# Optimization experiments

Hardware: AMD Instinct MI355X
Metric: run time of the kernel (lower is better)

Reference implementation:

```python
import jax, jax.numpy as jnp
import numpy as np

N = 100000  # nodes
E = 1600000  # edges

def gcn_layer(x, W, b, src, tgt, ew):
    # support = x @ W + b ; messages gathered at src, weighted scatter-sum into tgt
    h = x @ W + b                      # [N, F_out]
    msg = h[src] * ew[:, None]         # [E, F_out]
    return jax.ops.segment_sum(msg, tgt, num_segments=N)  # [N, F_out]

def setup_inputs() -> dict:
    key = jax.random.key(0)
    ks = jax.random.split(key, 12)
    nfeat, nhid, nclass = 256, 128, 40
    x = jax.random.normal(ks[0], (N, nfeat), dtype=jnp.float32)
    src = jax.random.randint(ks[1], (E,), 0, N)
    tgt = jax.random.randint(ks[2], (E,), 0, N)
    edge_weight = jax.random.uniform(ks[3], (E,), dtype=jnp.float32)
    def w(k, fi, fo):
        return jax.random.normal(k, (fi, fo), dtype=jnp.float32) / np.sqrt(fi)
    return {
        "x": x, "src": src, "tgt": tgt, "edge_weight": edge_weight,
        "W0": w(ks[4], nfeat, nhid), "b0": jnp.zeros((nhid,), jnp.float32),
        "W1": w(ks[5], nhid, nhid),  "b1": jnp.zeros((nhid,), jnp.float32),
        "W2": w(ks[6], nhid, nhid),  "b2": jnp.zeros((nhid,), jnp.float32),
        "W3": w(ks[7], nhid, nclass),"b3": jnp.zeros((nclass,), jnp.float32),
    }

def reference(x, src, tgt, edge_weight, W0, b0, W1, b1, W2, b2, W3, b3):
    # RESK2 with nlayers=4, eval mode (dropout = identity).
    # x0 = relu(gc0); r = x0; x1 = relu(gc1); x2 = relu(gc2) + r; out = log_softmax(gc3)
    x0 = jax.nn.relu(gcn_layer(x, W0, b0, src, tgt, edge_weight))
    r = x0
    x1 = jax.nn.relu(gcn_layer(x0, W1, b1, src, tgt, edge_weight))
    x2 = jax.nn.relu(gcn_layer(x1, W2, b2, src, tgt, edge_weight)) + r
    logits = gcn_layer(x2, W3, b3, src, tgt, edge_weight)
    return jax.nn.log_softmax(logits, axis=1)
```

## Files before the change

kernel.cpp:

```cpp
#include <hip/hip_runtime.h>
#include <hip/hip_bf16.h>


typedef __attribute__((ext_vector_type(8))) short short8;
typedef __attribute__((ext_vector_type(4))) float float4v;

#define SC_SHIFT 8
#define SC_NODES 256
#define FILL_CAP 12288
#define SRC_MASK 0x1FFFF

static __device__ __forceinline__ float bf2f_lo(unsigned int v) {
    return __uint_as_float(v << 16);
}
static __device__ __forceinline__ float bf2f_hi(unsigned int v) {
    return __uint_as_float(v & 0xffff0000u);
}
static __device__ __forceinline__ unsigned short f2bf(float f) {
    unsigned int u = __float_as_uint(f);
    u = (u + 0x7fffu + ((u >> 16) & 1u)) >> 16;
    return (unsigned short)u;
}
static __device__ __forceinline__ unsigned int packbf(float a, float b) {
    return (unsigned int)f2bf(a) | ((unsigned int)f2bf(b) << 16);
}
static __device__ __forceinline__ float pw_w(unsigned int pe) {
    return __uint_as_float((pe >> 17) << 16);
}

static __device__ __forceinline__ void acc8(float* acc, uint4 v, float wt) {
    acc[0] = fmaf(bf2f_lo(v.x), wt, acc[0]);
    acc[1] = fmaf(bf2f_hi(v.x), wt, acc[1]);
    acc[2] = fmaf(bf2f_lo(v.y), wt, acc[2]);
    acc[3] = fmaf(bf2f_hi(v.y), wt, acc[3]);
    acc[4] = fmaf(bf2f_lo(v.z), wt, acc[4]);
    acc[5] = fmaf(bf2f_hi(v.z), wt, acc[5]);
    acc[6] = fmaf(bf2f_lo(v.w), wt, acc[6]);
    acc[7] = fmaf(bf2f_hi(v.w), wt, acc[7]);
}
static __device__ __forceinline__ void acc4(float* acc, uint2 v, float wt) {
    acc[0] = fmaf(bf2f_lo(v.x), wt, acc[0]);
    acc[1] = fmaf(bf2f_hi(v.x), wt, acc[1]);
    acc[2] = fmaf(bf2f_lo(v.y), wt, acc[2]);
    acc[3] = fmaf(bf2f_hi(v.y), wt, acc[3]);
}

__global__ __launch_bounds__(256) void k_count(const int* __restrict__ tgt,
                                               int* __restrict__ chunkTot,
                                               int E, int NSC) {
    __shared__ int hist[512];
    const int tid = threadIdx.x;
    hist[tid] = 0;
    hist[tid + 256] = 0;
    __syncthreads();
#pragma unroll
    for (int r = 0; r < 4; r++) {
        int e = blockIdx.x * 4096 + r * 1024 + tid * 4;
        if (e + 3 < E) {
            int4 tv = *(const int4*)&tgt[e];
            atomicAdd(&hist[tv.x >> SC_SHIFT], 1);
            atomicAdd(&hist[tv.y >> SC_SHIFT], 1);
            atomicAdd(&hist[tv.z >> SC_SHIFT], 1);
            atomicAdd(&hist[tv.w >> SC_SHIFT], 1);
        } else {
            for (int j = 0; j < 4; j++)
                if (e + j < E) atomicAdd(&hist[tgt[e + j] >> SC_SHIFT], 1);
        }
    }
    __syncthreads();
    for (int i = tid; i < NSC; i += 256) {
        int c = hist[i];
        if (c) atomicAdd(&chunkTot[i], c);
    }
}

__global__ __launch_bounds__(512) void k_scanB(const int* __restrict__ chunkTot,
                                               int* __restrict__ chunkStart,
                                               int* __restrict__ chunkCur,
                                               int E, int NSC) {
    __shared__ int sm[512];
    const int tid = threadIdx.x;
    int v = (tid < NSC) ? chunkTot[tid] : 0;
    sm[tid] = v;
    __syncthreads();
    for (int off = 1; off < 512; off <<= 1) {
        int t = (tid >= off) ? sm[tid - off] : 0;
        __syncthreads();
        sm[tid] += t;
        __syncthreads();
    }
    int excl = sm[tid] - v;
    if (tid < NSC) {
        chunkStart[tid] = excl;
        chunkCur[tid * 32] = excl;
    }
    if (tid == 0) chunkStart[NSC] = E;
}

__global__ __launch_bounds__(512) void k_bucket(const int* __restrict__ src,
                                                const int* __restrict__ tgt,
                                                const float* __restrict__ ew,
                                                int* __restrict__ chunkCur,
                                                unsigned int* __restrict__ st_pw,
                                                unsigned char* __restrict__ st_t8,
                                                int E) {
    __shared__ int cnt[512];
    __shared__ int rk[512];
    __shared__ int bbase[512];
    const int tid = threadIdx.x;
    cnt[tid] = 0;
    rk[tid] = 0;
    __syncthreads();

    int t16[16];
    unsigned int p16[16];
#pragma unroll
    for (int r = 0; r < 4; r++) {
        int e = blockIdx.x * 8192 + r * 2048 + tid * 4;
        if (e + 3 < E) {
            int4 tv = *(const int4*)&tgt[e];
            int4 sv = *(const int4*)&src[e];
            float4 wv = *(const float4*)&ew[e];
            t16[r * 4 + 0] = tv.x; t16[r * 4 + 1] = tv.y;
            t16[r * 4 + 2] = tv.z; t16[r * 4 + 3] = tv.w;
            p16[r * 4 + 0] = ((unsigned int)f2bf(wv.x) << 17) | (unsigned int)sv.x;
            p16[r * 4 + 1] = ((unsigned int)f2bf(wv.y) << 17) | (unsigned int)sv.y;
            p16[r * 4 + 2] = ((unsigned int)f2bf(wv.z) << 17) | (unsigned int)sv.z;
            p16[r * 4 + 3] = ((unsigned int)f2bf(wv.w) << 17) | (unsigned int)sv.w;
        } else {
            for (int j = 0; j < 4; j++) {
                int ee = e + j;
                t16[r * 4 + j] = (ee < E) ? tgt[ee] : -1;
                p16[r * 4 + j] = (ee < E)
                    ? (((unsigned int)f2bf(ew[ee]) << 17) | (unsigned int)src[ee])
                    : 0u;
            }
        }
    }
#pragma unroll
    for (int j = 0; j < 16; j++)
        if (t16[j] >= 0) atomicAdd(&cnt[t16[j] >> SC_SHIFT], 1);
    __syncthreads();
    {
        int c = cnt[tid];
        bbase[tid] = c ? atomicAdd(&chunkCur[tid * 32], c) : 0;
    }
    __syncthreads();
#pragma unroll
    for (int j = 0; j < 16; j++) {
        if (t16[j] >= 0) {
            int c = t16[j] >> SC_SHIFT;
            int pos = bbase[c] + atomicAdd(&rk[c], 1);
            st_pw[pos] = p16[j];
            st_t8[pos] = (unsigned char)(t16[j] & (SC_NODES - 1));
        }
    }
}

__global__ __launch_bounds__(256) void k_fill2(const unsigned int* __restrict__ st_pw,
                                               const unsigned char* __restrict__ st_t8,
                                               const int* __restrict__ chunkStart,
                                               int* __restrict__ rowptr,
                                               unsigned int* __restrict__ perm,
                                               int N, int E, int NSC) {
    __shared__ int lhist[SC_NODES];
    __shared__ int lcur[SC_NODES];
    __shared__ unsigned int ledge[FILL_CAP];
    const int tid = threadIdx.x;
    const int b = blockIdx.x;
    const int n0 = b << SC_SHIFT;
    const int nlocal = min(SC_NODES, N - n0);
    const int sstart = chunkStart[b];
    const int send = chunkStart[b + 1];
    const int cnt = send - sstart;

    lhist[tid] = 0;
    __syncthreads();
    for (int e = sstart + tid; e < send; e += 256)
        atomicAdd(&lhist[st_t8[e]], 1);
    __syncthreads();
    int v = lhist[tid];
    __syncthreads();
    lhist[tid] = v;
    __syncthreads();
    for (int off = 1; off < 256; off <<= 1) {
        int t = (tid >= off) ? lhist[tid - off] : 0;
        __syncthreads();
        lhist[tid] += t;
        __syncthreads();
    }
    int excl = lhist[tid] - v;
    if (tid < nlocal) rowptr[n0 + tid] = sstart + excl;
    if (b == NSC - 1 && tid == 0) rowptr[N] = E;
    lcur[tid] = excl;
    __syncthreads();

    if (cnt <= FILL_CAP) {
        for (int e = sstart + tid; e < send; e += 256) {
            int lt = st_t8[e];
            int pos = atomicAdd(&lcur[lt], 1);
            ledge[pos] = st_pw[e];
        }
        __syncthreads();
        for (int i = tid; i < cnt; i += 256) perm[sstart + i] = ledge[i];
    } else {
        for (int e = sstart + tid; e < send; e += 256) {
            int lt = st_t8[e];
            int pos = atomicAdd(&lcur[lt], 1);
            perm[sstart + pos] = st_pw[e];
        }
    }
}

__global__ __launch_bounds__(256) void k_wtrans_all(
    const float* __restrict__ W0, const float* __restrict__ W1,
    const float* __restrict__ W2, const float* __restrict__ W3,
    unsigned short* __restrict__ Wt0, unsigned short* __restrict__ Wt1,
    unsigned short* __restrict__ Wt2, unsigned short* __restrict__ Wt3,
    int* __restrict__ chunkTot) {
    int idx = blockIdx.x * 256 + threadIdx.x;
    if (idx < 512) chunkTot[idx] = 0;
    if (idx < 32768) {
        int c = idx >> 8, k = idx & 255;
        Wt0[idx] = f2bf(W0[k * 128 + c]);
    } else if (idx < 49152) {
        int i = idx - 32768;
        int c = i >> 7, k = i & 127;
        Wt1[i] = f2bf(W1[k * 128 + c]);
    } else if (idx < 65536) {
        int i = idx - 49152;
        int c = i >> 7, k = i & 127;
        Wt2[i] = f2bf(W2[k * 128 + c]);
    } else if (idx < 71680) {
        int i = idx - 65536;
        int c = i >> 7, k = i & 127;
        Wt3[i] = (c < 40) ? f2bf(W3[k * 40 + c]) : 0;
    }
}

template <int K, int AF32>
__global__ __launch_bounds__(256) void k_gemm_mfma(const void* __restrict__ Av,
                                                   const unsigned short* __restrict__ Wt,
                                                   const float* __restrict__ bias,
                                                   unsigned short* __restrict__ C, int N) {
    __shared__ unsigned short As[128 * 40];
    __shared__ unsigned short Bs[128 * 40];
    __shared__ float bsh[128];
    const unsigned short* A16 = (const unsigned short*)Av;
    const float* A32 = (const float*)Av;
    const int tid = threadIdx.x;
    const int wave = tid >> 6, lane = tid & 63;
    const int quad = lane >> 4, l15 = lane & 15;
    const int rowBase = blockIdx.x * 128;

    if (tid < 128) bsh[tid] = bias[tid];

    const int r0 = tid >> 2, kc0 = tid & 3;
    const int r1 = (256 + tid) >> 2, kc1 = kc0;
    int rg0 = rowBase + r0; rg0 = rg0 < N ? rg0 : N - 1;
    int rg1 = rowBase + r1; rg1 = rg1 < N ? rg1 : N - 1;

    uint4 pa[2], pb[2];
    auto load_step = [&](int k0) {
        if (AF32) {
            float4 f0 = *(const float4*)&A32[(size_t)rg0 * K + k0 + kc0 * 8];
            float4 f1 = *(const float4*)&A32[(size_t)rg0 * K + k0 + kc0 * 8 + 4];
            pa[0].x = packbf(f0.x, f0.y); pa[0].y = packbf(f0.z, f0.w);
            pa[0].z = packbf(f1.x, f1.y); pa[0].w = packbf(f1.z, f1.w);
            float4 g0 = *(const float4*)&A32[(size_t)rg1 * K + k0 + kc1 * 8];
            float4 g1 = *(const float4*)&A32[(size_t)rg1 * K + k0 + kc1 * 8 + 4];
            pa[1].x = packbf(g0.x, g0.y); pa[1].y = packbf(g0.z, g0.w);
            pa[1].z = packbf(g1.x, g1.y); pa[1].w = packbf(g1.z, g1.w);
        } else {
            pa[0] = *(const uint4*)&A16[(size_t)rg0 * K + k0 + kc0 * 8];
            pa[1] = *(const uint4*)&A16[(size_t)rg1 * K + k0 + kc1 * 8];
        }
        pb[0] = *(const uint4*)&Wt[(size_t)r0 * K + k0 + kc0 * 8];
        pb[1] = *(const uint4*)&Wt[(size_t)r1 * K + k0 + kc1 * 8];
    };

    const float4v z = {0.f, 0.f, 0.f, 0.f};
    float4v acc[2][8];
#pragma unroll
    for (int i = 0; i < 2; i++)
#pragma unroll
        for (int j = 0; j < 8; j++) acc[i][j] = z;

    load_step(0);
    for (int k0 = 0; k0 < K; k0 += 32) {
        *(uint4*)&As[r0 * 40 + kc0 * 8] = pa[0];
        *(uint4*)&As[r1 * 40 + kc1 * 8] = pa[1];
        *(uint4*)&Bs[r0 * 40 + kc0 * 8] = pb[0];
        *(uint4*)&Bs[r1 * 40 + kc1 * 8] = pb[1];
        __syncthreads();
        if (k0 + 32 < K) load_step(k0 + 32);

        short8 a0 = *(const short8*)&As[(wave * 32 + l15) * 40 + quad * 8];
        short8 a1 = *(const short8*)&As[(wave * 32 + 16 + l15) * 40 + quad * 8];
#pragma unroll
        for (int c = 0; c < 8; c++) {
            short8 b = *(const short8*)&Bs[(c * 16 + l15) * 40 + quad * 8];
            acc[0][c] = __builtin_amdgcn_mfma_f32_16x16x32_bf16(b, a0, acc[0][c], 0, 0, 0);
            acc[1][c] = __builtin_amdgcn_mfma_f32_16x16x32_bf16(b, a1, acc[1][c], 0, 0, 0);
        }
        __syncthreads();
    }

#pragma unroll
    for (int rt = 0; rt < 2; rt++) {
        int row = rowBase + wave * 32 + rt * 16 + l15;
        if (row < N) {
#pragma unroll
            for (int c = 0; c < 8; c++) {
                int colBase = c * 16 + quad * 4;
                float4 bv = *(const float4*)&bsh[colBase];
                uint2 o;
                o.x = packbf(acc[rt][c][0] + bv.x, acc[rt][c][1] + bv.y);
                o.y = packbf(acc[rt][c][2] + bv.z, acc[rt][c][3] + bv.w);
                *(uint2*)&C[(size_t)row * 128 + colBase] = o;
            }
        }
    }
}

__global__ __launch_bounds__(256) void k_gemm40_mfma(const unsigned short* __restrict__ A,
                                                     const unsigned short* __restrict__ Wt3,
                                                     const float* __restrict__ bias,
                                                     unsigned short* __restrict__ C, int N) {
    __shared__ unsigned short As[128 * 40];
    __shared__ unsigned short Bs[48 * 136];
    __shared__ float bsh[48];
    const int tid = threadIdx.x;
    const int wave = tid >> 6, lane = tid & 63;
    const int quad = lane >> 4, l15 = lane & 15;
    const int rowBase = blockIdx.x * 128;

    if (tid < 48) bsh[tid] = (tid < 40) ? bias[tid] : 0.f;
    for (int t = tid; t < 48 * 16; t += 256) {
        int r = t >> 4, kc = t & 15;
        uint4 v = *(const uint4*)&Wt3[r * 128 + kc * 8];
        *(uint4*)&Bs[r * 136 + kc * 8] = v;
    }

    const int r0 = tid >> 2, kc0 = tid & 3;
    const int r1 = r0 + 64;
    int rg0 = rowBase + r0; rg0 = rg0 < N ? rg0 : N - 1;
    int rg1 = rowBase + r1; rg1 = rg1 < N ? rg1 : N - 1;

    uint4 pa[2];
    auto load_step = [&](int k0) {
        pa[0] = *(const uint4*)&A[(size_t)rg0 * 128 + k0 + kc0 * 8];
        pa[1] = *(const uint4*)&A[(size_t)rg1 * 128 + k0 + kc0 * 8];
    };

    const float4v z = {0.f, 0.f, 0.f, 0.f};
    float4v acc[2][3];
#pragma unroll
    for (int i = 0; i < 2; i++)
#pragma unroll
        for (int j = 0; j < 3; j++) acc[i][j] = z;

    load_step(0);
    for (int k0 = 0; k0 < 128; k0 += 32) {
        *(uint4*)&As[r0 * 40 + kc0 * 8] = pa[0];
        *(uint4*)&As[r1 * 40 + kc0 * 8] = pa[1];
        __syncthreads();
        if (k0 + 32 < 128) load_step(k0 + 32);

        short8 a0 = *(const short8*)&As[(wave * 32 + l15) * 40 + quad * 8];
        short8 a1 = *(const short8*)&As[(wave * 32 + 16 + l15) * 40 + quad * 8];
#pragma unroll
        for (int c = 0; c < 3; c++) {
            short8 b = *(const short8*)&Bs[(c * 16 + l15) * 136 + k0 + quad * 8];
            acc[0][c] = __builtin_amdgcn_mfma_f32_16x16x32_bf16(b, a0, acc[0][c], 0, 0, 0);
            acc[1][c] = __builtin_amdgcn_mfma_f32_16x16x32_bf16(b, a1, acc[1][c], 0, 0, 0);
        }
        __syncthreads();
    }

#pragma unroll
    for (int rt = 0; rt < 2; rt++) {
        int row = rowBase + wave * 32 + rt * 16 + l15;
        if (row < N) {
#pragma unroll
            for (int c = 0; c < 3; c++) {
                int colBase = c * 16 + quad * 4;
                float4 bv = *(const float4*)&bsh[colBase];
                uint2 o;
                o.x = packbf(acc[rt][c][0] + bv.x, acc[rt][c][1] + bv.y);
                o.y = packbf(acc[rt][c][2] + bv.z, acc[rt][c][3] + bv.w);
                *(uint2*)&C[(size_t)row * 64 + colBase] = o;
            }
        }
    }
}

__global__ __launch_bounds__(256) void k_agg128(const unsigned short* __restrict__ h,
                                                const int* __restrict__ rowptr,
                                                const unsigned int* __restrict__ perm,
                                                const unsigned short* __restrict__ resid,
                                                unsigned short* __restrict__ out, int N) {
    int node = (blockIdx.x * 256 + threadIdx.x) >> 6;
    if (node >= N) return;
    const int lane = threadIdx.x & 63;
    const int g = lane >> 4, l = lane & 15;
    const int beg = rowptr[node], end = rowptr[node + 1];
    const int last = end - 1;

    float acc[8] = {};
    for (int base = beg; base < end; base += 16) {
        int e0 = base + g, e1 = base + 4 + g, e2 = base + 8 + g, e3 = base + 12 + g;
        unsigned int p0 = perm[e0 <= last ? e0 : last];
        unsigned int p1 = perm[e1 <= last ? e1 : last];
        unsigned int p2 = perm[e2 <= last ? e2 : last];
        unsigned int p3 = perm[e3 <= last ? e3 : last];
        uint4 a0 = *(const uint4*)&h[(size_t)(p0 & SRC_MASK) * 128 + l * 8];
        uint4 a1 = *(const uint4*)&h[(size_t)(p1 & SRC_MASK) * 128 + l * 8];
        uint4 a2 = *(const uint4*)&h[(size_t)(p2 & SRC_MASK) * 128 + l * 8];
        uint4 a3 = *(const uint4*)&h[(size_t)(p3 & SRC_MASK) * 128 + l * 8];
        float w0 = e0 <= last ? pw_w(p0) : 0.f;
        float w1 = e1 <= last ? pw_w(p1) : 0.f;
        float w2 = e2 <= last ? pw_w(p2) : 0.f;
        float w3 = e3 <= last ? pw_w(p3) : 0.f;
        acc8(acc, a0, w0);
        acc8(acc, a1, w1);
        acc8(acc, a2, w2);
        acc8(acc, a3, w3);
    }

#pragma unroll
    for (int i = 0; i < 8; i++) {
        acc[i] += __shfl_xor(acc[i], 16);
        acc[i] += __shfl_xor(acc[i], 32);
    }

    if (g == 0) {
#pragma unroll
        for (int i = 0; i < 8; i++) acc[i] = fmaxf(acc[i], 0.f);
        if (resid) {
            uint4 rv = *(const uint4*)&resid[(size_t)node * 128 + l * 8];
            acc[0] += bf2f_lo(rv.x); acc[1] += bf2f_hi(rv.x);
            acc[2] += bf2f_lo(rv.y); acc[3] += bf2f_hi(rv.y);
            acc[4] += bf2f_lo(rv.z); acc[5] += bf2f_hi(rv.z);
            acc[6] += bf2f_lo(rv.w); acc[7] += bf2f_hi(rv.w);
        }
        uint4 o;
        o.x = packbf(acc[0], acc[1]);
        o.y = packbf(acc[2], acc[3]);
        o.z = packbf(acc[4], acc[5]);
        o.w = packbf(acc[6], acc[7]);
        *(uint4*)&out[(size_t)node * 128 + l * 8] = o;
    }
}

__global__ __launch_bounds__(256) void k_agg40_lsm(const unsigned short* __restrict__ h,
                                                   const int* __restrict__ rowptr,
                                                   const unsigned int* __restrict__ perm,
                                                   float* __restrict__ out, int N) {
    int node = (blockIdx.x * 256 + threadIdx.x) >> 6;
    if (node >= N) return;
    const int lane = threadIdx.x & 63;
    const int g = lane >> 4, l = lane & 15;
    const int beg = rowptr[node], end = rowptr[node + 1];
    const int last = end - 1;
    const int lc = l < 10 ? l : 0;

    float acc[4] = {};
    for (int base = beg; base < end; base += 16) {
        int e0 = base + g, e1 = base + 4 + g, e2 = base + 8 + g, e3 = base + 12 + g;
        unsigned int p0 = perm[e0 <= last ? e0 : last];
        unsigned int p1 = perm[e1 <= last ? e1 : last];
        unsigned int p2 = perm[e2 <= last ? e2 : last];
        unsigned int p3 = perm[e3 <= last ? e3 : last];
        uint2 a0 = *(const uint2*)&h[(size_t)(p0 & SRC_MASK) * 64 + lc * 4];
        uint2 a1 = *(const uint2*)&h[(size_t)(p1 & SRC_MASK) * 64 + lc * 4];
        uint2 a2 = *(const uint2*)&h[(size_t)(p2 & SRC_MASK) * 64 + lc * 4];
        uint2 a3 = *(const uint2*)&h[(size_t)(p3 & SRC_MASK) * 64 + lc * 4];
        float w0 = e0 <= last ? pw_w(p0) : 0.f;
        float w1 = e1 <= last ? pw_w(p1) : 0.f;
        float w2 = e2 <= last ? pw_w(p2) : 0.f;
        float w3 = e3 <= last ? pw_w(p3) : 0.f;
        acc4(acc, a0, w0);
        acc4(acc, a1, w1);
        acc4(acc, a2, w2);
        acc4(acc, a3, w3);
    }
#pragma unroll
    for (int i = 0; i < 4; i++) {
        acc[i] += __shfl_xor(acc[i], 16);
        acc[i] += __shfl_xor(acc[i], 32);
    }

    bool vf = l < 10;
    float m = vf ? fmaxf(fmaxf(acc[0], acc[1]), fmaxf(acc[2], acc[3]))
                 : -__builtin_inff();
#pragma unroll
    for (int off = 1; off < 16; off <<= 1) m = fmaxf(m, __shfl_xor(m, off));
    float s = vf ? (expf(acc[0] - m) + expf(acc[1] - m) +
                    expf(acc[2] - m) + expf(acc[3] - m))
                 : 0.f;
#pragma unroll
    for (int off = 1; off < 16; off <<= 1) s += __shfl_xor(s, off);
    float ls = m + logf(s);
    if (g == 0 && vf) {
        float4 o = make_float4(acc[0] - ls, acc[1] - ls, acc[2] - ls, acc[3] - ls);
        *(float4*)&out[(size_t)node * 40 + l * 4] = o;
    }
}

extern "C" void kernel_launch(void* const* d_in, const int* in_sizes, int n_in,
                              void* d_out, int out_size, void* d_ws, size_t ws_size,
                              hipStream_t stream) {
    const float* x  = (const float*)d_in[0];
    const int*   src = (const int*)d_in[1];
    const int*   tgt = (const int*)d_in[2];
    const float* ew  = (const float*)d_in[3];
    const float* W0 = (const float*)d_in[4];
    const float* b0 = (const float*)d_in[5];
    const float* W1 = (const float*)d_in[6];
    const float* b1 = (const float*)d_in[7];
    const float* W2 = (const float*)d_in[8];
    const float* b2 = (const float*)d_in[9];
    const float* W3 = (const float*)d_in[10];
    const float* b3 = (const float*)d_in[11];

    const int N = in_sizes[0] / 256;
    const int E = in_sizes[1];
    const int NSC = (N + SC_NODES - 1) >> SC_SHIFT;

    char* ws = (char*)d_ws;
    size_t off = 0;
    auto alloc = [&](size_t bytes) -> void* {
        void* p = ws + off;
        off = (off + bytes + 255) & ~(size_t)255;
        return p;
    };
    unsigned short* XCb = (unsigned short*)alloc((size_t)N * 128 * 2);
    size_t hbytes = (size_t)N * 128 * 2;
    size_t sbytes = (size_t)E * 5 + 256;
    char* hbuf = (char*)alloc(hbytes > sbytes ? hbytes : sbytes);
    unsigned short* Hb = (unsigned short*)hbuf;
    unsigned int* st_pw = (unsigned int*)hbuf;
    unsigned char* st_t8 = (unsigned char*)(hbuf + (size_t)E * 4);
    char* buf1 = (char*)alloc((size_t)N * 128 * 2);
    unsigned short* XAb  = (unsigned short*)buf1;
    unsigned short* H40b = (unsigned short*)buf1;
    unsigned short* XBb  = (unsigned short*)alloc((size_t)N * 128 * 2);
    int*   rowptr    = (int*)alloc((size_t)(N + 1) * 4);
    int*   chunkTot  = (int*)alloc(512 * 4);
    int*   chunkStart= (int*)alloc(520 * 4);
    int*   chunkCur  = (int*)alloc(512 * 32 * 4);
    unsigned int* perm = (unsigned int*)alloc((size_t)E * 4);
    unsigned short* Wt0 = (unsigned short*)alloc(256 * 128 * 2);
    unsigned short* Wt1 = (unsigned short*)alloc(128 * 128 * 2);
    unsigned short* Wt2 = (unsigned short*)alloc(128 * 128 * 2);
    unsigned short* Wt3 = (unsigned short*)alloc(48 * 128 * 2);
    (void)ws_size;

    float* logits = (float*)d_out;

    k_wtrans_all<<<(71680 + 255) / 256, 256, 0, stream>>>(W0, W1, W2, W3,
                                                          Wt0, Wt1, Wt2, Wt3,
                                                          chunkTot);
    k_count<<<(E + 4095) / 4096, 256, 0, stream>>>(tgt, chunkTot, E, NSC);
    k_scanB<<<1, 512, 0, stream>>>(chunkTot, chunkStart, chunkCur, E, NSC);
    k_bucket<<<(E + 8191) / 8192, 512, 0, stream>>>(src, tgt, ew, chunkCur,
                                                    st_pw, st_t8, E);
    k_fill2<<<NSC, 256, 0, stream>>>(st_pw, st_t8, chunkStart, rowptr, perm,
                                     N, E, NSC);

    const int gGemm = (N + 127) / 128;
    const int gWave = (N + 3) / 4;

    k_gemm_mfma<256, 1><<<gGemm, 256, 0, stream>>>(x, Wt0, b0, Hb, N);
    k_agg128<<<gWave, 256, 0, stream>>>(Hb, rowptr, perm, nullptr, XAb, N);
    k_gemm_mfma<128, 0><<<gGemm, 256, 0, stream>>>(XAb, Wt1, b1, Hb, N);
    k_agg128<<<gWave, 256, 0, stream>>>(Hb, rowptr, perm, nullptr, XBb, N);
    k_gemm_mfma<128, 0><<<gGemm, 256, 0, stream>>>(XBb, Wt2, b2, Hb, N);
    k_agg128<<<gWave, 256, 0, stream>>>(Hb, rowptr, perm, XAb, XCb, N);
    k_gemm40_mfma<<<gGemm, 256, 0, stream>>>(XCb, Wt3, b3, H40b, N);
    k_agg40_lsm<<<gWave, 256, 0, stream>>>(H40b, rowptr, perm, logits, N);
}
```

Baseline: 548.2 us.

## Halve GEMM row tile to 64 and stage output through LDS for coalesced stores

```diff
diff --git a/kernel.cpp b/kernel.cpp
--- a/kernel.cpp
+++ b/kernel.cpp
@@ -243,82 +243,84 @@
                                                    const unsigned short* __restrict__ Wt,
                                                    const float* __restrict__ bias,
                                                    unsigned short* __restrict__ C, int N) {
-    __shared__ unsigned short As[128 * 40];
-    __shared__ unsigned short Bs[128 * 40];
+    __shared__ union {
+        struct {
+            unsigned short As[64 * 40];
+            unsigned short Bs[128 * 40];
+        } s;
+        unsigned short Cs[64 * 136];
+    } u;
     __shared__ float bsh[128];
     const unsigned short* A16 = (const unsigned short*)Av;
     const float* A32 = (const float*)Av;
     const int tid = threadIdx.x;
     const int wave = tid >> 6, lane = tid & 63;
     const int quad = lane >> 4, l15 = lane & 15;
-    const int rowBase = blockIdx.x * 128;
+    const int rowBase = blockIdx.x * 64;
 
     if (tid < 128) bsh[tid] = bias[tid];
 
     const int r0 = tid >> 2, kc0 = tid & 3;
-    const int r1 = (256 + tid) >> 2, kc1 = kc0;
-    int rg0 = rowBase + r0; rg0 = rg0 < N ? rg0 : N - 1;
-    int rg1 = rowBase + r1; rg1 = rg1 < N ? rg1 : N - 1;
-
-    uint4 pa[2], pb[2];
+    const int rB1 = r0, rB2 = r0 + 64;
+    int rg0 = rowBase + r0;
+    rg0 = rg0 < N ? rg0 : N - 1;
+
+    uint4 pa, pb0, pb1;
     auto load_step = [&](int k0) {
         if (AF32) {
             float4 f0 = *(const float4*)&A32[(size_t)rg0 * K + k0 + kc0 * 8];
             float4 f1 = *(const float4*)&A32[(size_t)rg0 * K + k0 + kc0 * 8 + 4];
-            pa[0].x = packbf(f0.x, f0.y); pa[0].y = packbf(f0.z, f0.w);
-            pa[0].z = packbf(f1.x, f1.y); pa[0].w = packbf(f1.z, f1.w);
-            float4 g0 = *(const float4*)&A32[(size_t)rg1 * K + k0 + kc1 * 8];
-            float4 g1 = *(const float4*)&A32[(size_t)rg1 * K + k0 + kc1 * 8 + 4];
-            pa[1].x = packbf(g0.x, g0.y); pa[1].y = packbf(g0.z, g0.w);
-            pa[1].z = packbf(g1.x, g1.y); pa[1].w = packbf(g1.z, g1.w);
+            pa.x = packbf(f0.x, f0.y);
+            pa.y = packbf(f0.z, f0.w);
+            pa.z = packbf(f1.x, f1.y);
+            pa.w = packbf(f1.z, f1.w);
         } else {
-            pa[0] = *(const uint4*)&A16[(size_t)rg0 * K + k0 + kc0 * 8];
-            pa[1] = *(const uint4*)&A16[(size_t)rg1 * K + k0 + kc1 * 8];
-        }
-        pb[0] = *(const uint4*)&Wt[(size_t)r0 * K + k0 + kc0 * 8];
-        pb[1] = *(const uint4*)&Wt[(size_t)r1 * K + k0 + kc1 * 8];
+            pa = *(const uint4*)&A16[(size_t)rg0 * K + k0 + kc0 * 8];
+        }
+        pb0 = *(const uint4*)&Wt[(size_t)rB1 * K + k0 + kc0 * 8];
+        pb1 = *(const uint4*)&Wt[(size_t)rB2 * K + k0 + kc0 * 8];
     };
 
     const float4v z = {0.f, 0.f, 0.f, 0.f};
-    float4v acc[2][8];
-#pragma unroll
-    for (int i = 0; i < 2; i++)
-#pragma unroll
-        for (int j = 0; j < 8; j++) acc[i][j] = z;
+    float4v acc[8];
+#pragma unroll
+    for (int j = 0; j < 8; j++) acc[j] = z;
 
     load_step(0);
     for (int k0 = 0; k0 < K; k0 += 32) {
-        *(uint4*)&As[r0 * 40 + kc0 * 8] = pa[0];
-        *(uint4*)&As[r1 * 40 + kc1 * 8] = pa[1];
-        *(uint4*)&Bs[r0 * 40 + kc0 * 8] = pb[0];
-        *(uint4*)&Bs[r1 * 40 + kc1 * 8] = pb[1];
+        *(uint4*)&u.s.As[r0 * 40 + kc0 * 8] = pa;
+        *(uint4*)&u.s.Bs[rB1 * 40 + kc0 * 8] = pb0;
+        *(uint4*)&u.s.Bs[rB2 * 40 + kc0 * 8] = pb1;
         __syncthreads();
         if (k0 + 32 < K) load_step(k0 + 32);
 
-        short8 a0 = *(const short8*)&As[(wave * 32 + l15) * 40 + quad * 8];
-        short8 a1 = *(const short8*)&As[(wave * 32 + 16 + l15) * 40 + quad * 8];
+        short8 a = *(const short8*)&u.s.As[(wave * 16 + l15) * 40 + quad * 8];
 #pragma unroll
         for (int c = 0; c < 8; c++) {
-            short8 b = *(const short8*)&Bs[(c * 16 + l15) * 40 + quad * 8];
-            acc[0][c] = __builtin_amdgcn_mfma_f32_16x16x32_bf16(b, a0, acc[0][c], 0, 0, 0);
-            acc[1][c] = __builtin_amdgcn_mfma_f32_16x16x32_bf16(b, a1, acc[1][c], 0, 0, 0);
-        }
-        __syncthreads();
-    }
-
-#pragma unroll
-    for (int rt = 0; rt < 2; rt++) {
-        int row = rowBase + wave * 32 + rt * 16 + l15;
-        if (row < N) {
-#pragma unroll
-            for (int c = 0; c < 8; c++) {
-                int colBase = c * 16 + quad * 4;
-                float4 bv = *(const float4*)&bsh[colBase];
-                uint2 o;
-                o.x = packbf(acc[rt][c][0] + bv.x, acc[rt][c][1] + bv.y);
-                o.y = packbf(acc[rt][c][2] + bv.z, acc[rt][c][3] + bv.w);
-                *(uint2*)&C[(size_t)row * 128 + colBase] = o;
-            }
+            short8 b = *(const short8*)&u.s.Bs[(c * 16 + l15) * 40 + quad * 8];
+            acc[c] = __builtin_amdgcn_mfma_f32_16x16x32_bf16(b, a, acc[c], 0, 0, 0);
+        }
+        __syncthreads();
+    }
+
+#pragma unroll
+    for (int c = 0; c < 8; c++) {
+        int colBase = c * 16 + quad * 4;
+        float4 bv = *(const float4*)&bsh[colBase];
+        uint2 o;
+        o.x = packbf(acc[c][0] + bv.x, acc[c][1] + bv.y);
+        o.y = packbf(acc[c][2] + bv.z, acc[c][3] + bv.w);
+        *(uint2*)&u.Cs[(wave * 16 + l15) * 136 + colBase] = o;
+    }
+    __syncthreads();
+#pragma unroll
+    for (int i = 0; i < 4; i++) {
+        int flat = i * 256 + tid;
+        int row = flat >> 4, q = flat & 15;
+        int grow = rowBase + row;
+        if (grow < N) {
+            uint4 v = *(const uint4*)&u.Cs[row * 136 + q * 8];
+            *(uint4*)&C[(size_t)grow * 128 + q * 8] = v;
         }
     }
 }
@@ -327,70 +329,79 @@
                                                      const unsigned short* __restrict__ Wt3,
                                                      const float* __restrict__ bias,
                                                      unsigned short* __restrict__ C, int N) {
-    __shared__ unsigned short As[128 * 40];
-    __shared__ unsigned short Bs[48 * 136];
-    __shared__ float bsh[48];
+    __shared__ union {
+        struct {
+            unsigned short As[64 * 40];
+            unsigned short Bs[48 * 136];
+        } s;
+        unsigned short Cs[64 * 72];
+    } u;
+    __shared__ float bsh[64];
     const int tid = threadIdx.x;
     const int wave = tid >> 6, lane = tid & 63;
     const int quad = lane >> 4, l15 = lane & 15;
-    const int rowBase = blockIdx.x * 128;
-
-    if (tid < 48) bsh[tid] = (tid < 40) ? bias[tid] : 0.f;
+    const int rowBase = blockIdx.x * 64;
+
+    if (tid < 64) bsh[tid] = (tid < 40) ? bias[tid] : 0.f;
+
+    const int r0 = tid >> 2, kc0 = tid & 3;
+    int rg0 = rowBase + r0;
+    rg0 = rg0 < N ? rg0 : N - 1;
+
     for (int t = tid; t < 48 * 16; t += 256) {
         int r = t >> 4, kc = t & 15;
         uint4 v = *(const uint4*)&Wt3[r * 128 + kc * 8];
-        *(uint4*)&Bs[r * 136 + kc * 8] = v;
-    }
-
-    const int r0 = tid >> 2, kc0 = tid & 3;
-    const int r1 = r0 + 64;
-    int rg0 = rowBase + r0; rg0 = rg0 < N ? rg0 : N - 1;
-    int rg1 = rowBase + r1; rg1 = rg1 < N ? rg1 : N - 1;
-
-    uint4 pa[2];
+        *(uint4*)&u.s.Bs[r * 136 + kc * 8] = v;
+    }
+
+    uint4 pa;
     auto load_step = [&](int k0) {
-        pa[0] = *(const uint4*)&A[(size_t)rg0 * 128 + k0 + kc0 * 8];
-        pa[1] = *(const uint4*)&A[(size_t)rg1 * 128 + k0 + kc0 * 8];
+        pa = *(const uint4*)&A[(size_t)rg0 * 128 + k0 + kc0 * 8];
     };
 
     const float4v z = {0.f, 0.f, 0.f, 0.f};
-    float4v acc[2][3];
-#pragma unroll
-    for (int i = 0; i < 2; i++)
-#pragma unroll
-        for (int j = 0; j < 3; j++) acc[i][j] = z;
+    float4v acc[3];
+#pragma unroll
+    for (int j = 0; j < 3; j++) acc[j] = z;
 
     load_step(0);
     for (int k0 = 0; k0 < 128; k0 += 32) {
-        *(uint4*)&As[r0 * 40 + kc0 * 8] = pa[0];
-        *(uint4*)&As[r1 * 40 + kc0 * 8] = pa[1];
+        *(uint4*)&u.s.As[r0 * 40 + kc0 * 8] = pa;
         __syncthreads();
         if (k0 + 32 < 128) load_step(k0 + 32);
 
-        short8 a0 = *(const short8*)&As[(wave * 32 + l15) * 40 + quad * 8];
-        short8 a1 = *(const short8*)&As[(wave * 32 + 16 + l15) * 40 + quad * 8];
+        short8 a = *(const short8*)&u.s.As[(wave * 16 + l15) * 40 + quad * 8];
 #pragma unroll
         for (int c = 0; c < 3; c++) {
-            short8 b = *(const short8*)&Bs[(c * 16 + l15) * 136 + k0 + quad * 8];
-            acc[0][c] = __builtin_amdgcn_mfma_f32_16x16x32_bf16(b, a0, acc[0][c], 0, 0, 0);
-            acc[1][c] = __builtin_amdgcn_mfma_f32_16x16x32_bf16(b, a1, acc[1][c], 0, 0, 0);
-        }
-        __syncthreads();
-    }
-
-#pragma unroll
-    for (int rt = 0; rt < 2; rt++) {
-        int row = rowBase + wave * 32 + rt * 16 + l15;
-        if (row < N) {
-#pragma unroll
-            for (int c = 0; c < 3; c++) {
-                int colBase = c * 16 + quad * 4;
-                float4 bv = *(const float4*)&bsh[colBase];
-                uint2 o;
-                o.x = packbf(acc[rt][c][0] + bv.x, acc[rt][c][1] + bv.y);
-                o.y = packbf(acc[rt][c][2] + bv.z, acc[rt][c][3] + bv.w);
-                *(uint2*)&C[(size_t)row * 64 + colBase] = o;
-            }
+            short8 b = *(const short8*)&u.s.Bs[(c * 16 + l15) * 136 + k0 + quad * 8];
+            acc[c] = __builtin_amdgcn_mfma_f32_16x16x32_bf16(b, a, acc[c], 0, 0, 0);
+        }
+        __syncthreads();
+    }
+
+#pragma unroll
+    for (int c = 0; c < 4; c++) {
+        int colBase = c * 16 + quad * 4;
+        uint2 o;
+        if (c < 3) {
+            float4 bv = *(const float4*)&bsh[colBase];
+            o.x = packbf(acc[c][0] + bv.x, acc[c][1] + bv.y);
+            o.y = packbf(acc[c][2] + bv.z, acc[c][3] + bv.w);
+        } else {
+            o.x = 0u;
+            o.y = 0u;
+        }
+        *(uint2*)&u.Cs[(wave * 16 + l15) * 72 + colBase] = o;
+    }
+    __syncthreads();
+#pragma unroll
+    for (int i = 0; i < 2; i++) {
+        int flat = i * 256 + tid;
+        int row = flat >> 3, q = flat & 7;
+        int grow = rowBase + row;
+        if (grow < N) {
+            uint4 v = *(const uint4*)&u.Cs[row * 72 + q * 8];
+            *(uint4*)&C[(size_t)grow * 64 + q * 8] = v;
         }
     }
 }
@@ -569,7 +580,7 @@
     k_fill2<<<NSC, 256, 0, stream>>>(st_pw, st_t8, chunkStart, rowptr, perm,
                                      N, E, NSC);
 
-    const int gGemm = (N + 127) / 128;
+    const int gGemm = (N + 63) / 64;
     const int gWave = (N + 3) / 4;
 
     k_gemm_mfma<256, 1><<<gGemm, 256, 0, stream>>>(x, Wt0, b0, Hb, N);
```

Result: faster. 490.6 us (-10.5%).
